# Kernel optimization log

Measured on AMD Instinct MI355X. Metric: run time of the kernel, lower is better.

## Reference

```python
import jax, jax.numpy as jnp
import numpy as np

B, S, D, H, F = 4, 2048, 1024, 16, 4096
HD = D // H
EPS = 1e-4


def setup_inputs() -> dict:
    key = jax.random.key(0)
    ks = jax.random.split(key, 10)
    sd = 1.0 / np.sqrt(D)
    sf = 1.0 / np.sqrt(F)
    return {
        "x":  jax.random.normal(ks[0], (B, S, D), dtype=jnp.float32),
        "wq": jax.random.uniform(ks[1], (D, D), jnp.float32, -sd, sd),
        "wk": jax.random.uniform(ks[2], (D, D), jnp.float32, -sd, sd),
        "wv": jax.random.uniform(ks[3], (D, D), jnp.float32, -sd, sd),
        "wu": jax.random.uniform(ks[4], (D, D), jnp.float32, -sd, sd),
        "bu": jax.random.uniform(ks[5], (D,), jnp.float32, -sd, sd),
        "w1": jax.random.uniform(ks[6], (F, D), jnp.float32, -sd, sd),
        "b1": jax.random.uniform(ks[7], (F,), jnp.float32, -sd, sd),
        "w2": jax.random.uniform(ks[8], (D, F), jnp.float32, -sf, sf),
        "b2": jax.random.uniform(ks[9], (D,), jnp.float32, -sf, sf),
    }


def _ln(x):
    # LN with gamma=1, beta=0 (module initializes them to ones/zeros)
    mean = jnp.mean(x, axis=-1, keepdims=True)
    var = jnp.mean((x - mean) ** 2, axis=-1, keepdims=True)
    return (x - mean) / jnp.sqrt(var + EPS)


def _mhsa(x, wq, wk, wv, wu, bu):
    b, s, d = x.shape
    # torch Linear: y = x @ W.T
    q = (x @ wq.T).reshape(b, s, H, HD).transpose(0, 2, 1, 3)  # bhsd
    k = (x @ wk.T).reshape(b, s, H, HD).transpose(0, 2, 1, 3)
    v = (x @ wv.T).reshape(b, s, H, HD).transpose(0, 2, 1, 3)
    scores = jnp.einsum("bhqd,bhkd->bhqk", q, k) / jnp.sqrt(jnp.float32(HD))
    causal = jnp.triu(jnp.ones((s, s), dtype=bool), k=1)
    scores = jnp.where(causal, -jnp.inf, scores)
    attn = jax.nn.softmax(scores, axis=-1)
    ctx = jnp.einsum("bhqk,bhkd->bhqd", attn, v)
    ctx = ctx.transpose(0, 2, 1, 3).reshape(b, s, d)
    return ctx @ wu.T + bu


def reference(x, wq, wk, wv, wu, bu, w1, b1, w2, b2):
    attn = _mhsa(_ln(x), wq, wk, wv, wu, bu)
    h = x + attn
    ff = jax.nn.relu(_ln(h) @ w1.T + b1) @ w2.T + b2
    return h + ff
```

## Files before the change

kernel.cpp:

```cpp
#include <hip/hip_runtime.h>
#include <hip/hip_bf16.h>
#include <stdint.h>

#define BB   4
#define SS   2048
#define DD   1024
#define NH   16
#define HDIM 64
#define FF   4096
#define NROW (BB*SS)
#define LN_EPS 1e-4f

typedef __attribute__((ext_vector_type(8))) short  bf16x8;
typedef __attribute__((ext_vector_type(4))) float  f32x4;

__device__ __forceinline__ ushort f2bf(float f) {
    uint32_t u = __builtin_bit_cast(uint32_t, f);
    u += 0x7fff + ((u >> 16) & 1);
    return (ushort)(u >> 16);
}

__device__ __forceinline__ void load_lds16(const void* g, void* l) {
    __builtin_amdgcn_global_load_lds(
        (const __attribute__((address_space(1))) void*)g,
        (__attribute__((address_space(3))) void*)l, 16, 0, 0);
}

__global__ __launch_bounds__(256) void cvt_all(
    const float* __restrict__ wq, const float* __restrict__ wk,
    const float* __restrict__ wv, const float* __restrict__ wu,
    const float* __restrict__ w1, const float* __restrict__ w2,
    ushort* __restrict__ wqkv, ushort* __restrict__ wu_b,
    ushort* __restrict__ w1_b, ushort* __restrict__ w2_b) {
    int i = blockIdx.x * 256 + threadIdx.x;
    const float* src; ushort* dst; int off;
    if (i < 262144)       { src = wq; dst = wqkv;           off = i; }
    else if (i < 524288)  { src = wk; dst = wqkv + 1048576; off = i - 262144; }
    else if (i < 786432)  { src = wv; dst = wqkv + 2097152; off = i - 524288; }
    else if (i < 1048576) { src = wu; dst = wu_b;           off = i - 786432; }
    else if (i < 2097152) { src = w1; dst = w1_b;           off = i - 1048576; }
    else                  { src = w2; dst = w2_b;           off = i - 2097152; }
    float4 v = ((const float4*)src)[off];
    ushort4 o;
    o.x = f2bf(v.x); o.y = f2bf(v.y); o.z = f2bf(v.z); o.w = f2bf(v.w);
    ((ushort4*)dst)[off] = o;
}

__global__ __launch_bounds__(256) void ln_kernel(const float* __restrict__ x,
                                                 ushort* __restrict__ out) {
    int row = blockIdx.x;
    const float4* xr = (const float4*)(x + (size_t)row * DD);
    float4 v = xr[threadIdx.x];
    float s  = v.x + v.y + v.z + v.w;
    float ss = v.x*v.x + v.y*v.y + v.z*v.z + v.w*v.w;
    #pragma unroll
    for (int o = 32; o; o >>= 1) {
        s  += __shfl_xor(s, o);
        ss += __shfl_xor(ss, o);
    }
    __shared__ float ps[4], pss[4];
    if ((threadIdx.x & 63) == 0) { ps[threadIdx.x >> 6] = s; pss[threadIdx.x >> 6] = ss; }
    __syncthreads();
    s  = ps[0] + ps[1] + ps[2] + ps[3];
    ss = pss[0] + pss[1] + pss[2] + pss[3];
    float mean = s * (1.0f / DD);
    float var  = ss * (1.0f / DD) - mean * mean;
    float rstd = rsqrtf(var + LN_EPS);
    ushort4 o4;
    o4.x = f2bf((v.x - mean) * rstd);
    o4.y = f2bf((v.y - mean) * rstd);
    o4.z = f2bf((v.z - mean) * rstd);
    o4.w = f2bf((v.w - mean) * rstd);
    ((ushort4*)(out + (size_t)row * DD))[threadIdx.x] = o4;
}

template<int MODE>
__global__ __launch_bounds__(256, 2) void gemm_bt(
    const ushort* __restrict__ A, const ushort* __restrict__ B,
    void* __restrict__ C, const float* __restrict__ bias,
    const float* __restrict__ resid, int M, int N, int K)
{
    __shared__ ushort As[128 * 32];
    __shared__ ushort Bs[128 * 32];

    int nn  = N >> 7;
    int nwg = (M >> 7) * nn;
    int bid = blockIdx.x;
    int wg  = (bid & 7) * (nwg >> 3) + (bid >> 3);
    int tm = wg / nn, tn = wg % nn;
    size_t m0 = (size_t)tm * 128, n0 = (size_t)tn * 128;

    int tid = threadIdx.x, w = tid >> 6, lane = tid & 63;
    int lq = lane & 15, g = lane >> 4;
    int wr = w >> 1, wc = w & 1;

    f32x4 acc[4][4] = {};

    const int f0 = w * 1024 + lane * 8;

    for (int k0 = 0; k0 < K; k0 += 32) {
        __syncthreads();
        #pragma unroll
        for (int i = 0; i < 2; i++) {
            int f = f0 + i * 512;
            int r = f >> 5, c = f & 31;
            load_lds16(A + (m0 + r) * K + k0 + c, As + w * 1024 + i * 512);
            load_lds16(B + (n0 + r) * K + k0 + c, Bs + w * 1024 + i * 512);
        }
        __syncthreads();

        bf16x8 a[4], b[4];
        #pragma unroll
        for (int mt = 0; mt < 4; mt++)
            a[mt] = *(const bf16x8*)&As[(wr * 64 + mt * 16 + lq) * 32 + g * 8];
        #pragma unroll
        for (int nt = 0; nt < 4; nt++)
            b[nt] = *(const bf16x8*)&Bs[(wc * 64 + nt * 16 + lq) * 32 + g * 8];
        #pragma unroll
        for (int mt = 0; mt < 4; mt++)
            #pragma unroll
            for (int nt = 0; nt < 4; nt++)
                acc[mt][nt] = __builtin_amdgcn_mfma_f32_16x16x32_bf16(
                    a[mt], b[nt], acc[mt][nt], 0, 0, 0);
    }

    #pragma unroll
    for (int mt = 0; mt < 4; mt++) {
        #pragma unroll
        for (int nt = 0; nt < 4; nt++) {
            #pragma unroll
            for (int r = 0; r < 4; r++) {
                size_t row = m0 + wr * 64 + mt * 16 + g * 4 + r;
                size_t col = n0 + wc * 64 + nt * 16 + lq;
                float v = acc[mt][nt][r];
                if (MODE == 0) {
                    ((ushort*)C)[row * N + col] = f2bf(v);
                } else if (MODE == 1) {
                    ((float*)C)[row * N + col] = v + bias[col] + resid[row * N + col];
                } else {
                    float t = v + bias[col];
                    ((ushort*)C)[row * N + col] = f2bf(t > 0.f ? t : 0.f);
                }
            }
        }
    }
}

#define MFMA_BF16 __builtin_amdgcn_mfma_f32_16x16x32_bf16

template<int MODE>
__global__ __launch_bounds__(512, 2) void gemm256(
    const ushort* __restrict__ Aw, const ushort* __restrict__ Bw,
    void* __restrict__ C, const float* __restrict__ bias,
    int M, int N, int K)
{
    __shared__ ushort Ls[2][4][8192];

    int nn  = N >> 8;
    int nwg = (M >> 8) * nn;
    int bid = blockIdx.x;
    int wg  = (bid & 7) * (nwg >> 3) + (bid >> 3);
    int tm = wg / nn, tn = wg % nn;
    size_t m0 = (size_t)tm * 256, n0 = (size_t)tn * 256;

    int tid = threadIdx.x, wid = tid >> 6, lane = tid & 63;
    int lq = lane & 15, g = lane >> 4;
    int wr = wid >> 2, wc = wid & 3;

    f32x4 acc[8][4] = {};

#define STG(Tn, h, dbuf) do {                                                   \
    int ks_ = (h) >> 1;                                                         \
    const ushort* s_ = ((h) & 1) ? (Bw + n0 * (size_t)K) : (Aw + m0 * (size_t)K); \
    int kk_ = (Tn) * 64 + ks_ * 32;                                             \
    { int F_ = tid;       int r_ = F_ >> 2, c_ = F_ & 3;                        \
      load_lds16(s_ + (size_t)r_ * K + kk_ + ((c_ ^ ((r_ >> 1) & 3)) * 8),      \
                 &Ls[dbuf][h][(wid * 64) * 8]); }                               \
    { int F_ = 512 + tid; int r_ = F_ >> 2, c_ = F_ & 3;                        \
      load_lds16(s_ + (size_t)r_ * K + kk_ + ((c_ ^ ((r_ >> 1) & 3)) * 8),      \
                 &Ls[dbuf][h][(512 + wid * 64) * 8]); }                         \
  } while (0)

#define RD_A(mt, ks) (*(const bf16x8*)&Ls[cur][(ks)*2][((wr*128 + (mt)*16 + lq) * 32) + ((g ^ (((wr*128 + (mt)*16 + lq) >> 1) & 3)) * 8)])
#define RD_B(nt, ks) (*(const bf16x8*)&Ls[cur][(ks)*2+1][((wc*64 + (nt)*16 + lq) * 32) + ((g ^ (((wc*64 + (nt)*16 + lq) >> 1) & 3)) * 8)])

    STG(0, 0, 0); STG(0, 1, 0); STG(0, 2, 0); STG(0, 3, 0);
    asm volatile("s_waitcnt vmcnt(4)" ::: "memory");
    __builtin_amdgcn_sched_barrier(0);
    __builtin_amdgcn_s_barrier();

    int KT = K >> 6;
    #pragma unroll 1
    for (int T = 0; T < KT; ++T) {
        int cur = T & 1;
        bool st = (T + 1 < KT);
        bf16x8 aF[8], bF[4];

        #pragma unroll
        for (int mt = 0; mt < 8; mt++) aF[mt] = RD_A(mt, 0);
        bF[0] = RD_B(0, 0); bF[1] = RD_B(1, 0);
        if (st) STG(T + 1, 0, cur ^ 1);
        __builtin_amdgcn_s_barrier();
        asm volatile("s_waitcnt lgkmcnt(0)" ::: "memory");
        __builtin_amdgcn_sched_barrier(0);
        __builtin_amdgcn_s_setprio(1);
        #pragma unroll
        for (int mt = 0; mt < 8; mt++) {
            acc[mt][0] = MFMA_BF16(aF[mt], bF[0], acc[mt][0], 0, 0, 0);
            acc[mt][1] = MFMA_BF16(aF[mt], bF[1], acc[mt][1], 0, 0, 0);
        }
        __builtin_amdgcn_s_setprio(0);
        __builtin_amdgcn_s_barrier();

        bF[2] = RD_B(2, 0); bF[3] = RD_B(3, 0);
        if (st) STG(T + 1, 1, cur ^ 1);
        __builtin_amdgcn_s_barrier();
        asm volatile("s_waitcnt lgkmcnt(0)" ::: "memory");
        __builtin_amdgcn_sched_barrier(0);
        __builtin_amdgcn_s_setprio(1);
        #pragma unroll
        for (int mt = 0; mt < 8; mt++) {
            acc[mt][2] = MFMA_BF16(aF[mt], bF[2], acc[mt][2], 0, 0, 0);
            acc[mt][3] = MFMA_BF16(aF[mt], bF[3], acc[mt][3], 0, 0, 0);
        }
        __builtin_amdgcn_s_setprio(0);
        if (st) asm volatile("s_waitcnt vmcnt(4)" ::: "memory");
        else    asm volatile("s_waitcnt vmcnt(0)" ::: "memory");
        __builtin_amdgcn_sched_barrier(0);
        __builtin_amdgcn_s_barrier();

        #pragma unroll
        for (int mt = 0; mt < 8; mt++) aF[mt] = RD_A(mt, 1);
        bF[0] = RD_B(0, 1); bF[1] = RD_B(1, 1);
        if (st) STG(T + 1, 2, cur ^ 1);
        __builtin_amdgcn_s_barrier();
        asm volatile("s_waitcnt lgkmcnt(0)" ::: "memory");
        __builtin_amdgcn_sched_barrier(0);
        __builtin_amdgcn_s_setprio(1);
        #pragma unroll
        for (int mt = 0; mt < 8; mt++) {
            acc[mt][0] = MFMA_BF16(aF[mt], bF[0], acc[mt][0], 0, 0, 0);
            acc[mt][1] = MFMA_BF16(aF[mt], bF[1], acc[mt][1], 0, 0, 0);
        }
        __builtin_amdgcn_s_setprio(0);
        __builtin_amdgcn_s_barrier();

        bF[2] = RD_B(2, 1); bF[3] = RD_B(3, 1);
        if (st) STG(T + 1, 3, cur ^ 1);
        __builtin_amdgcn_s_barrier();
        asm volatile("s_waitcnt lgkmcnt(0)" ::: "memory");
        __builtin_amdgcn_sched_barrier(0);
        __builtin_amdgcn_s_setprio(1);
        #pragma unroll
        for (int mt = 0; mt < 8; mt++) {
            acc[mt][2] = MFMA_BF16(aF[mt], bF[2], acc[mt][2], 0, 0, 0);
            acc[mt][3] = MFMA_BF16(aF[mt], bF[3], acc[mt][3], 0, 0, 0);
        }
        __builtin_amdgcn_s_setprio(0);
        if (st) {
            asm volatile("s_waitcnt vmcnt(4)" ::: "memory");
            __builtin_amdgcn_sched_barrier(0);
        }
        __builtin_amdgcn_s_barrier();
    }

    #pragma unroll
    for (int mt = 0; mt < 8; mt++) {
        #pragma unroll
        for (int nt = 0; nt < 4; nt++) {
            #pragma unroll
            for (int r = 0; r < 4; r++) {
                size_t row = m0 + wr * 128 + mt * 16 + g * 4 + r;
                size_t col = n0 + wc * 64 + nt * 16 + lq;
                float v = acc[mt][nt][r];
                if (MODE == 0) {
                    ((ushort*)C)[row * N + col] = f2bf(v);
                } else {
                    float t = v + bias[col];
                    ((ushort*)C)[row * N + col] = f2bf(t > 0.f ? t : 0.f);
                }
            }
        }
    }
#undef STG
#undef RD_A
#undef RD_B
}

__global__ __launch_bounds__(256) void transpose_v(const ushort* __restrict__ qkv,
                                                   ushort* __restrict__ vt) {
    int idx = blockIdx.x * 256 + threadIdx.x;
    int s   = idx & (SS - 1);
    int cg  = (idx >> 11) & 7;
    int bh  = idx >> 14;
    int b = bh >> 4, h = bh & 15;
    bf16x8 v = *(const bf16x8*)(qkv + ((size_t)b * SS + s) * 3072 + 2048 + h * 64 + cg * 8);
    #pragma unroll
    for (int j = 0; j < 8; j++)
        vt[((size_t)bh * 64 + cg * 8 + j) * SS + s] = ((ushort*)&v)[j];
}

__global__ __launch_bounds__(256, 3) void attn_kernel(const ushort* __restrict__ qkv,
                                                      const ushort* __restrict__ vt,
                                                      ushort* __restrict__ ctx) {
    __shared__ ushort   Kl[2][64 * 64];
    __shared__ ushort   Vl[2][64 * 64];
    __shared__ uint32_t Pl[4][32 * 20];

    int pr = blockIdx.x;
    int bh = blockIdx.y;
    int b = bh >> 4, h = bh & 15;
    int tid = threadIdx.x, wid = tid >> 6, lane = tid & 63;
    int lq = lane & 15, g = lane >> 4;
    int sr = tid >> 3;
    int sc = (tid & 7) * 8;
    const float CE = 0.125f * 1.44269504f;

    const ushort* kbase = qkv + (size_t)b * SS * 3072 + 1024 + h * 64;
    const ushort* vbase = vt + (size_t)bh * 64 * SS;

    #define LOADSTAGE(T) do { int k0_ = (T) * 64;                                   \
        kr0 = *(const bf16x8*)(kbase + (size_t)(k0_ + sr) * 3072 + sc);             \
        kr1 = *(const bf16x8*)(kbase + (size_t)(k0_ + 32 + sr) * 3072 + sc);        \
        vr0 = *(const bf16x8*)(vbase + (size_t)sr * SS + k0_ + sc);                 \
        vr1 = *(const bf16x8*)(vbase + (size_t)(32 + sr) * SS + k0_ + sc); } while (0)

    #define WRITESTAGE(BUF) do {                                                    \
        int r0_ = sr, r1_ = 32 + sr, cc_ = sc >> 3;                                 \
        *(bf16x8*)&Kl[BUF][r0_ * 64 + ((cc_ ^ (r0_ & 7)) << 3)] = kr0;              \
        *(bf16x8*)&Kl[BUF][r1_ * 64 + ((cc_ ^ (r1_ & 7)) << 3)] = kr1;              \
        *(bf16x8*)&Vl[BUF][r0_ * 64 + ((cc_ ^ (r0_ & 7)) << 3)] = vr0;              \
        *(bf16x8*)&Vl[BUF][r1_ * 64 + ((cc_ ^ (r1_ & 7)) << 3)] = vr1; } while (0)

    #pragma unroll 1
    for (int half = 0; half < 2; half++) {
        int bx = half ? (31 - pr) : pr;
        int q0 = bx * 64;
        int qrow = q0 + wid * 16 + lq;
        const size_t qoff = ((size_t)b * SS + qrow) * 3072 + h * 64;
        bf16x8 qf0 = *(const bf16x8*)(qkv + qoff + g * 8);
        bf16x8 qf1 = *(const bf16x8*)(qkv + qoff + 32 + g * 8);

        f32x4 oacc[4] = {};
        float m = -1e30f, l = 0.f;
        int ntile = bx + 1;

        bf16x8 kr0, kr1, vr0, vr1;
        LOADSTAGE(0);
        __syncthreads();
        WRITESTAGE(0);
        int cur = 0;

        #pragma unroll 1
        for (int t = 0; t < ntile; ++t) {
            __syncthreads();
            if (t + 1 < ntile) LOADSTAGE(t + 1);

            f32x4 sa[4];
            __builtin_amdgcn_s_setprio(1);
            #pragma unroll
            for (int mt = 0; mt < 4; mt++) {
                int row = mt * 16 + lq;
                sa[mt] = f32x4{0.f, 0.f, 0.f, 0.f};
                bf16x8 a0 = *(const bf16x8*)&Kl[cur][row * 64 + ((g ^ (row & 7)) << 3)];
                sa[mt] = __builtin_amdgcn_mfma_f32_16x16x32_bf16(a0, qf0, sa[mt], 0, 0, 0);
                bf16x8 a1 = *(const bf16x8*)&Kl[cur][row * 64 + (((4 + g) ^ (row & 7)) << 3)];
                sa[mt] = __builtin_amdgcn_mfma_f32_16x16x32_bf16(a1, qf1, sa[mt], 0, 0, 0);
            }
            __builtin_amdgcn_s_setprio(0);

            float p[4][4];
            float tmax = -1e30f;
            if (t == ntile - 1) {
                int k0 = t * 64;
                #pragma unroll
                for (int mt = 0; mt < 4; mt++)
                    #pragma unroll
                    for (int r = 0; r < 4; r++) {
                        float s = sa[mt][r];
                        int key = k0 + mt * 16 + g * 4 + r;
                        if (key > qrow) s = -1e30f;
                        p[mt][r] = s;
                        tmax = fmaxf(tmax, s);
                    }
            } else {
                #pragma unroll
                for (int mt = 0; mt < 4; mt++)
                    #pragma unroll
                    for (int r = 0; r < 4; r++) {
                        float s = sa[mt][r];
                        p[mt][r] = s;
                        tmax = fmaxf(tmax, s);
                    }
            }
            tmax = fmaxf(tmax, __shfl_xor(tmax, 16));
            tmax = fmaxf(tmax, __shfl_xor(tmax, 32));
            float mnew  = fmaxf(m, tmax);
            float alpha = exp2f((m - mnew) * CE);
            float sum = 0.f;
            #pragma unroll
            for (int mt = 0; mt < 4; mt++)
                #pragma unroll
                for (int r = 0; r < 4; r++) {
                    float e = exp2f((p[mt][r] - mnew) * CE);
                    p[mt][r] = e;
                    sum += e;
                }
            sum += __shfl_xor(sum, 16);
            sum += __shfl_xor(sum, 32);
            l = l * alpha + sum;
            m = mnew;
            #pragma unroll
            for (int mt = 0; mt < 4; mt++)
                #pragma unroll
                for (int r = 0; r < 4; r++) oacc[mt][r] *= alpha;

            #pragma unroll
            for (int mt = 0; mt < 4; mt++)
                #pragma unroll
                for (int w2 = 0; w2 < 2; w2++) {
                    uint32_t pk = (uint32_t)f2bf(p[mt][2 * w2]) |
                                  ((uint32_t)f2bf(p[mt][2 * w2 + 1]) << 16);
                    Pl[wid][(mt * 8 + g * 2 + w2) * 20 + lq] = pk;
                }

            __builtin_amdgcn_s_setprio(1);
            #pragma unroll
            for (int ks = 0; ks < 2; ks++) {
                union { uint32_t w[4]; bf16x8 v; } pb;
                #pragma unroll
                for (int c = 0; c < 4; c++)
                    pb.w[c] = Pl[wid][(ks * 16 + g * 4 + c) * 20 + lq];
                #pragma unroll
                for (int mt = 0; mt < 4; mt++) {
                    int row = mt * 16 + lq;
                    bf16x8 af = *(const bf16x8*)&Vl[cur][row * 64 + (((ks * 4 + g) ^ (row & 7)) << 3)];
                    oacc[mt] = __builtin_amdgcn_mfma_f32_16x16x32_bf16(af, pb.v, oacc[mt], 0, 0, 0);
                }
            }
            __builtin_amdgcn_s_setprio(0);

            if (t + 1 < ntile) WRITESTAGE(cur ^ 1);
            cur ^= 1;
        }

        float inv = 1.f / l;
        ushort* cb = ctx + ((size_t)b * SS + qrow) * DD + h * 64;
        #pragma unroll
        for (int mt = 0; mt < 4; mt++)
            #pragma unroll
            for (int r = 0; r < 4; r++)
                cb[mt * 16 + g * 4 + r] = f2bf(oacc[mt][r] * inv);
    }
    #undef LOADSTAGE
    #undef WRITESTAGE
}

extern "C" void kernel_launch(void* const* d_in, const int* in_sizes, int n_in,
                              void* d_out, int out_size, void* d_ws, size_t ws_size,
                              hipStream_t stream) {
    const float* x  = (const float*)d_in[0];
    const float* wq = (const float*)d_in[1];
    const float* wk = (const float*)d_in[2];
    const float* wv = (const float*)d_in[3];
    const float* wu = (const float*)d_in[4];
    const float* bu = (const float*)d_in[5];
    const float* w1 = (const float*)d_in[6];
    const float* b1 = (const float*)d_in[7];
    const float* w2 = (const float*)d_in[8];
    const float* b2 = (const float*)d_in[9];
    float* out = (float*)d_out;

    ushort* ws = (ushort*)d_ws;
    size_t off = 0;
    ushort* wqkv = ws + off; off += (size_t)3072 * 1024;
    ushort* wu_b = ws + off; off += (size_t)1024 * 1024;
    ushort* w1_b = ws + off; off += (size_t)4096 * 1024;
    ushort* w2_b = ws + off; off += (size_t)4096 * 1024;
    ushort* lnb  = ws + off; off += (size_t)NROW * DD;
    float*  hbuf = (float*)(ws + off); off += (size_t)NROW * DD * 2;
    ushort* qkv  = ws + off;
    ushort* ctx  = qkv + (size_t)NROW * 3072;
    ushort* gbuf = qkv;
    off += (size_t)NROW * FF;
    ushort* vtb  = ws + off; off += (size_t)NROW * DD;
    (void)ws_size; (void)n_in; (void)in_sizes; (void)out_size;

    cvt_all<<<12288, 256, 0, stream>>>(wq, wk, wv, wu, w1, w2,
                                       wqkv, wu_b, w1_b, w2_b);

    ln_kernel<<<NROW, 256, 0, stream>>>(x, lnb);
    gemm256<0><<<(NROW / 256) * (3072 / 256), 512, 0, stream>>>(
        lnb, wqkv, qkv, nullptr, NROW, 3072, 1024);
    transpose_v<<<4096, 256, 0, stream>>>(qkv, vtb);
    attn_kernel<<<dim3(16, BB * NH), 256, 0, stream>>>(qkv, vtb, ctx);
    gemm_bt<1><<<(NROW / 128) * (1024 / 128), 256, 0, stream>>>(
        ctx, wu_b, hbuf, bu, x, NROW, 1024, 1024);
    ln_kernel<<<NROW, 256, 0, stream>>>(hbuf, lnb);
    gemm256<2><<<(NROW / 256) * (4096 / 256), 512, 0, stream>>>(
        lnb, w1_b, gbuf, b1, NROW, 4096, 1024);
    gemm_bt<1><<<(NROW / 128) * (1024 / 128), 256, 0, stream>>>(
        gbuf, w2_b, out, b2, hbuf, NROW, 1024, 4096);
}
```

Before: 516.6 us.

## Reorder GEMM MFMA fragments, lazy softmax rescale, hw bf16 pack, swap attention grid axes

```diff
diff --git a/kernel.cpp b/kernel.cpp
--- a/kernel.cpp
+++ b/kernel.cpp
@@ -194,35 +194,37 @@
     for (int T = 0; T < KT; ++T) {
         int cur = T & 1;
         bool st = (T + 1 < KT);
-        bf16x8 aF[8], bF[4];
-
-        #pragma unroll
-        for (int mt = 0; mt < 8; mt++) aF[mt] = RD_A(mt, 0);
-        bF[0] = RD_B(0, 0); bF[1] = RD_B(1, 0);
+        bf16x8 aF[4], bF[4];
+
+        #pragma unroll
+        for (int i = 0; i < 4; i++) aF[i] = RD_A(i, 0);
+        #pragma unroll
+        for (int i = 0; i < 4; i++) bF[i] = RD_B(i, 0);
         if (st) STG(T + 1, 0, cur ^ 1);
         __builtin_amdgcn_s_barrier();
         asm volatile("s_waitcnt lgkmcnt(0)" ::: "memory");
         __builtin_amdgcn_sched_barrier(0);
         __builtin_amdgcn_s_setprio(1);
         #pragma unroll
-        for (int mt = 0; mt < 8; mt++) {
-            acc[mt][0] = MFMA_BF16(aF[mt], bF[0], acc[mt][0], 0, 0, 0);
-            acc[mt][1] = MFMA_BF16(aF[mt], bF[1], acc[mt][1], 0, 0, 0);
-        }
+        for (int i = 0; i < 4; i++)
+            #pragma unroll
+            for (int nt = 0; nt < 4; nt++)
+                acc[i][nt] = MFMA_BF16(aF[i], bF[nt], acc[i][nt], 0, 0, 0);
         __builtin_amdgcn_s_setprio(0);
         __builtin_amdgcn_s_barrier();
 
-        bF[2] = RD_B(2, 0); bF[3] = RD_B(3, 0);
+        #pragma unroll
+        for (int i = 0; i < 4; i++) aF[i] = RD_A(4 + i, 0);
         if (st) STG(T + 1, 1, cur ^ 1);
         __builtin_amdgcn_s_barrier();
         asm volatile("s_waitcnt lgkmcnt(0)" ::: "memory");
         __builtin_amdgcn_sched_barrier(0);
         __builtin_amdgcn_s_setprio(1);
         #pragma unroll
-        for (int mt = 0; mt < 8; mt++) {
-            acc[mt][2] = MFMA_BF16(aF[mt], bF[2], acc[mt][2], 0, 0, 0);
-            acc[mt][3] = MFMA_BF16(aF[mt], bF[3], acc[mt][3], 0, 0, 0);
-        }
+        for (int i = 0; i < 4; i++)
+            #pragma unroll
+            for (int nt = 0; nt < 4; nt++)
+                acc[4 + i][nt] = MFMA_BF16(aF[i], bF[nt], acc[4 + i][nt], 0, 0, 0);
         __builtin_amdgcn_s_setprio(0);
         if (st) asm volatile("s_waitcnt vmcnt(4)" ::: "memory");
         else    asm volatile("s_waitcnt vmcnt(0)" ::: "memory");
@@ -230,32 +232,34 @@
         __builtin_amdgcn_s_barrier();
 
         #pragma unroll
-        for (int mt = 0; mt < 8; mt++) aF[mt] = RD_A(mt, 1);
-        bF[0] = RD_B(0, 1); bF[1] = RD_B(1, 1);
+        for (int i = 0; i < 4; i++) aF[i] = RD_A(i, 1);
+        #pragma unroll
+        for (int i = 0; i < 4; i++) bF[i] = RD_B(i, 1);
         if (st) STG(T + 1, 2, cur ^ 1);
         __builtin_amdgcn_s_barrier();
         asm volatile("s_waitcnt lgkmcnt(0)" ::: "memory");
         __builtin_amdgcn_sched_barrier(0);
         __builtin_amdgcn_s_setprio(1);
         #pragma unroll
-        for (int mt = 0; mt < 8; mt++) {
-            acc[mt][0] = MFMA_BF16(aF[mt], bF[0], acc[mt][0], 0, 0, 0);
-            acc[mt][1] = MFMA_BF16(aF[mt], bF[1], acc[mt][1], 0, 0, 0);
-        }
+        for (int i = 0; i < 4; i++)
+            #pragma unroll
+            for (int nt = 0; nt < 4; nt++)
+                acc[i][nt] = MFMA_BF16(aF[i], bF[nt], acc[i][nt], 0, 0, 0);
         __builtin_amdgcn_s_setprio(0);
         __builtin_amdgcn_s_barrier();
 
-        bF[2] = RD_B(2, 1); bF[3] = RD_B(3, 1);
+        #pragma unroll
+        for (int i = 0; i < 4; i++) aF[i] = RD_A(4 + i, 1);
         if (st) STG(T + 1, 3, cur ^ 1);
         __builtin_amdgcn_s_barrier();
         asm volatile("s_waitcnt lgkmcnt(0)" ::: "memory");
         __builtin_amdgcn_sched_barrier(0);
         __builtin_amdgcn_s_setprio(1);
         #pragma unroll
-        for (int mt = 0; mt < 8; mt++) {
-            acc[mt][2] = MFMA_BF16(aF[mt], bF[2], acc[mt][2], 0, 0, 0);
-            acc[mt][3] = MFMA_BF16(aF[mt], bF[3], acc[mt][3], 0, 0, 0);
-        }
+        for (int i = 0; i < 4; i++)
+            #pragma unroll
+            for (int nt = 0; nt < 4; nt++)
+                acc[4 + i][nt] = MFMA_BF16(aF[i], bF[nt], acc[4 + i][nt], 0, 0, 0);
         __builtin_amdgcn_s_setprio(0);
         if (st) {
             asm volatile("s_waitcnt vmcnt(4)" ::: "memory");
@@ -307,8 +311,8 @@
     __shared__ ushort   Vl[2][64 * 64];
     __shared__ uint32_t Pl[4][32 * 20];
 
-    int pr = blockIdx.x;
-    int bh = blockIdx.y;
+    int bh = blockIdx.x;
+    int pr = blockIdx.y;
     int b = bh >> 4, h = bh & 15;
     int tid = threadIdx.x, wid = tid >> 6, lane = tid & 63;
     int lq = lane & 15, g = lane >> 4;
@@ -395,32 +399,38 @@
             }
             tmax = fmaxf(tmax, __shfl_xor(tmax, 16));
             tmax = fmaxf(tmax, __shfl_xor(tmax, 32));
-            float mnew  = fmaxf(m, tmax);
-            float alpha = exp2f((m - mnew) * CE);
+
+            if (!__all(tmax - m <= 8.0f)) {
+                float mnew  = fmaxf(m, tmax);
+                float alpha = exp2f((m - mnew) * CE);
+                l *= alpha;
+                #pragma unroll
+                for (int mt = 0; mt < 4; mt++)
+                    #pragma unroll
+                    for (int r = 0; r < 4; r++) oacc[mt][r] *= alpha;
+                m = mnew;
+            }
+
             float sum = 0.f;
             #pragma unroll
             for (int mt = 0; mt < 4; mt++)
                 #pragma unroll
                 for (int r = 0; r < 4; r++) {
-                    float e = exp2f((p[mt][r] - mnew) * CE);
+                    float e = exp2f((p[mt][r] - m) * CE);
                     p[mt][r] = e;
                     sum += e;
                 }
             sum += __shfl_xor(sum, 16);
             sum += __shfl_xor(sum, 32);
-            l = l * alpha + sum;
-            m = mnew;
+            l += sum;
+
             #pragma unroll
             for (int mt = 0; mt < 4; mt++)
                 #pragma unroll
-                for (int r = 0; r < 4; r++) oacc[mt][r] *= alpha;
-
-            #pragma unroll
-            for (int mt = 0; mt < 4; mt++)
-                #pragma unroll
                 for (int w2 = 0; w2 < 2; w2++) {
-                    uint32_t pk = (uint32_t)f2bf(p[mt][2 * w2]) |
-                                  ((uint32_t)f2bf(p[mt][2 * w2 + 1]) << 16);
+                    uint32_t pk;
+                    asm("v_cvt_pk_bf16_f32 %0, %1, %2"
+                        : "=v"(pk) : "v"(p[mt][2 * w2]), "v"(p[mt][2 * w2 + 1]));
                     Pl[wid][(mt * 8 + g * 2 + w2) * 20 + lq] = pk;
                 }
 
@@ -493,7 +503,7 @@
     gemm256<0><<<(NROW / 256) * (3072 / 256), 512, 0, stream>>>(
         lnb, wqkv, qkv, nullptr, NROW, 3072, 1024);
     transpose_v<<<4096, 256, 0, stream>>>(qkv, vtb);
-    attn_kernel<<<dim3(16, BB * NH), 256, 0, stream>>>(qkv, vtb, ctx);
+    attn_kernel<<<dim3(BB * NH, 16), 256, 0, stream>>>(qkv, vtb, ctx);
     gemm_bt<1><<<(NROW / 128) * (1024 / 128), 256, 0, stream>>>(
         ctx, wu_b, hbuf, bu, x, NROW, 1024, 1024);
     ln_kernel<<<NROW, 256, 0, stream>>>(hbuf, lnb);
```

New measurement: 510.8 us. No clear change (-1.1%).
